# Performance work log

Hardware: AMD Instinct MI355X
Metric: run time of the kernel (lower is better)

The kernel has to match this reference:

```python
import jax, jax.numpy as jnp
import numpy as np

INF = 100000.0
B, W, T, U, S, N = 64, 16, 64, 128, 20, 8


def setup_inputs() -> dict:
    key = jax.random.key(0)
    ks = jax.random.split(key, 9)
    xavier = (2.0 / (U + U)) ** 0.5
    return {
        "slot_utt_h": jax.random.normal(ks[0], (B, W, T, U), jnp.float32),
        "slot_candidate_c": jax.random.normal(ks[1], (S, U), jnp.float32),
        "status_candidate_c": jax.random.normal(ks[2], (N, U), jnp.float32),
        "position_encoding": jax.random.normal(ks[3], (B, W, S, U), jnp.float32),
        "q_status": jax.random.normal(ks[4], (B, W, N, U), jnp.float32),
        "mask": jnp.zeros((B, W, S * N), jnp.float32),
        "weight": jax.random.normal(ks[5], (U, U), jnp.float32) * xavier,  # bilinear co-attention weight [U,U]
        "W1": jax.random.normal(ks[6], (2 * U, U), jnp.float32) * 0.05,
        "b1": jnp.zeros((U,), jnp.float32),
        "W2": jax.random.normal(ks[7], (U, U), jnp.float32) * 0.05,
        "b2": jnp.zeros((U,), jnp.float32),
        "W3": jax.random.normal(ks[8], (U, 1), jnp.float32) * 0.05,
        "b3": jnp.zeros((1,), jnp.float32),
    }


def _zero_mask(p):
    # original: -(p == 0).float() * INF, added before softmax
    return jnp.where(p == 0.0, -INF, 0.0)


def reference(slot_utt_h, slot_candidate_c, status_candidate_c, position_encoding,
              q_status, mask, weight, W1, b1, W2, b2, W3, b3):
    # ---- attention over utterance tokens ----
    # p[b,w,s,t] = <slot_candidate_c[s], slot_utt_h[b,w,t]>
    p = jnp.einsum('su,bwtu->bwst', slot_candidate_c, slot_utt_h)
    p = jax.nn.softmax(p + _zero_mask(p), axis=-1)
    q_slot = jnp.einsum('bwst,bwtu->bwsu', p, slot_utt_h) + position_encoding  # [B,W,S,U]

    # ---- bilinear co-attention: [B,W*S,U] @ weight @ [B,U,W*N] -> [B,W,S,W,N] ----
    co = jnp.einsum('bwsu,uv,bxnv->bwsxn', q_slot, weight, q_status)
    p2 = jax.nn.softmax(co + _zero_mask(co), axis=3)  # softmax over the second window axis x

    # weighted sum of statuses over window axis x
    q_status_slot = jnp.einsum('bwsxn,bxnu->bwsnu', p2, q_status)  # [B,W,S,N,U]

    q_slot_exp = jnp.broadcast_to(q_slot[:, :, :, None, :], (B, W, S, N, U))
    features = jnp.concatenate([q_slot_exp, q_status_slot], axis=-1)  # [B,W,S,N,2U]

    # ---- MLP (dropout in eval mode = identity) ----
    h = jax.nn.relu(features @ W1 + b1)
    h = jax.nn.relu(h @ W2 + b2)
    logits = h @ W3 + b3  # [B,W,S,N,1]

    logits = logits.reshape(B, W, S * N)
    slot_pred_logits = jnp.max(logits + mask, axis=1)  # masked max-pool over window
    slot_pred_labels = (slot_pred_logits > 0.0).astype(jnp.float32)
    return (slot_pred_labels, S * N, slot_pred_logits)
```

## Files before the change

kernel.cpp:

```cpp
#include <hip/hip_runtime.h>
#include <math.h>

#define INF_ 100000.0f
constexpr int B_ = 64, W_ = 16, T_ = 64, U_ = 128, S_ = 20, N_ = 8;

typedef unsigned short ushort_t;
typedef __attribute__((ext_vector_type(8))) short bf16x8;
typedef __attribute__((ext_vector_type(4))) float floatx4;

static __device__ __forceinline__ unsigned short f2bf(float x) {
    unsigned int u = __float_as_uint(x);
    return (unsigned short)((u + 0x7fff + ((u >> 16) & 1)) >> 16);
}
static __device__ __forceinline__ float bf2f(unsigned short s) {
    return __uint_as_float(((unsigned int)s) << 16);
}

#define HT_SWZ(u, t) ((u) * 72 + ((t) ^ ((((u) >> 3) & 7) << 3)))

__global__ __launch_bounds__(256) void k_pre(
    const float* __restrict__ q_status, const float* __restrict__ weight,
    const float* __restrict__ W1, const float* __restrict__ W2,
    const float* __restrict__ c,
    ushort_t* __restrict__ w1topT, ushort_t* __restrict__ w2T,
    ushort_t* __restrict__ c_bf,
    ushort_t* __restrict__ Gt_bf, ushort_t* __restrict__ qs1T_bf)
{
    __shared__ __align__(16) ushort_t sw[128 * 136];
    __shared__ __align__(16) ushort_t sq[128 * 136];
    const int tid = threadIdx.x, bx = blockIdx.x;

    if (bx < 64) {
        const int b = bx;
        const float* qb = q_status + (size_t)b * 16384;
        for (int i = tid * 4; i < 16384; i += 1024) {
            int r = i >> 7, v = i & 127;
            float4 wv = *(const float4*)&weight[i];
            *(ushort4*)&sw[r * 136 + v] =
                (ushort4){f2bf(wv.x), f2bf(wv.y), f2bf(wv.z), f2bf(wv.w)};
            float4 qv = *(const float4*)&qb[i];
            *(ushort4*)&sq[r * 136 + v] =
                (ushort4){f2bf(qv.x), f2bf(qv.y), f2bf(qv.z), f2bf(qv.w)};
        }
        __syncthreads();
        const int wave = tid >> 6, lane = tid & 63, m16 = lane & 15, q = lane >> 4;
        ushort_t* Gb = Gt_bf + (size_t)b * 16384;
#pragma unroll
        for (int ci = 0; ci < 16; ++ci) {
            int tile = wave * 16 + ci;
            int mt = tile >> 3, jt = tile & 7;
            floatx4 acc = {0.f, 0.f, 0.f, 0.f};
#pragma unroll
            for (int kt = 0; kt < 4; ++kt) {
                bf16x8 a = *(const bf16x8*)&sq[(mt * 16 + m16) * 136 + kt * 32 + q * 8];
                bf16x8 w = *(const bf16x8*)&sw[(jt * 16 + m16) * 136 + kt * 32 + q * 8];
                acc = __builtin_amdgcn_mfma_f32_16x16x32_bf16(a, w, acc, 0, 0, 0);
            }
#pragma unroll
            for (int reg = 0; reg < 4; ++reg)
                Gb[(mt * 16 + q * 4 + reg) * 128 + jt * 16 + m16] = f2bf(acc[reg]);
        }
        return;
    }
    if (bx < 128) {
        const int b = bx - 64;
        const float* qb = q_status + (size_t)b * 16384;
        for (int i = tid * 4; i < 16384; i += 1024) {
            int r = i >> 7, v = i & 127;
            float4 qv = *(const float4*)&qb[i];
            *(ushort4*)&sq[r * 136 + v] =
                (ushort4){f2bf(qv.x), f2bf(qv.y), f2bf(qv.z), f2bf(qv.w)};
            int v2 = i >> 7, j = i & 127;
            float4 wv = *(const float4*)&W1[(128 + v2) * 128 + j];
            sw[(j + 0) * 136 + v2] = f2bf(wv.x);
            sw[(j + 1) * 136 + v2] = f2bf(wv.y);
            sw[(j + 2) * 136 + v2] = f2bf(wv.z);
            sw[(j + 3) * 136 + v2] = f2bf(wv.w);
        }
        __syncthreads();
        const int wave = tid >> 6, lane = tid & 63, m16 = lane & 15, q = lane >> 4;
        ushort_t* Qb = qs1T_bf + (size_t)b * 16384;
#pragma unroll
        for (int ci = 0; ci < 16; ++ci) {
            int tile = wave * 16 + ci;
            int mt = tile >> 3, jt = tile & 7;
            floatx4 acc = {0.f, 0.f, 0.f, 0.f};
#pragma unroll
            for (int kt = 0; kt < 4; ++kt) {
                bf16x8 a = *(const bf16x8*)&sq[(mt * 16 + m16) * 136 + kt * 32 + q * 8];
                bf16x8 w = *(const bf16x8*)&sw[(jt * 16 + m16) * 136 + kt * 32 + q * 8];
                acc = __builtin_amdgcn_mfma_f32_16x16x32_bf16(a, w, acc, 0, 0, 0);
            }
            ushort4 o = {f2bf(acc[0]), f2bf(acc[1]), f2bf(acc[2]), f2bf(acc[3])};
            *(ushort4*)&Qb[(jt * 16 + m16) * 128 + mt * 16 + q * 4] = o;
        }
        return;
    }
    if (bx < 144) {
        int g = (bx - 128) * 1024 + tid * 4;
        int j = g >> 7, k = g & 127;
        *(ushort4*)&w1topT[g] =
            (ushort4){f2bf(W1[k * 128 + j]), f2bf(W1[(k + 1) * 128 + j]),
                      f2bf(W1[(k + 2) * 128 + j]), f2bf(W1[(k + 3) * 128 + j])};
        return;
    }
    if (bx < 160) {
        int g = (bx - 144) * 1024 + tid * 4;
        int j = g >> 7, k = g & 127;
        *(ushort4*)&w2T[g] =
            (ushort4){f2bf(W2[k * 128 + j]), f2bf(W2[(k + 1) * 128 + j]),
                      f2bf(W2[(k + 2) * 128 + j]), f2bf(W2[(k + 3) * 128 + j])};
        return;
    }
    for (int i = tid * 4; i < 4096; i += 1024) {
        int s = i >> 7;
        ushort4 o = {0, 0, 0, 0};
        if (s < 20) {
            float4 v = *(const float4*)&c[i];
            o = (ushort4){f2bf(v.x), f2bf(v.y), f2bf(v.z), f2bf(v.w)};
        }
        *(ushort4*)&c_bf[i] = o;
    }
}

__global__ __launch_bounds__(256) void kA(
    const float* __restrict__ h,
    const ushort_t* __restrict__ c_bf,
    const float* __restrict__ pos,
    ushort_t* __restrict__ q_slot_bf)
{
    __shared__ __align__(16) ushort_t sh_hT[128 * 72];
    __shared__ __align__(16) float    sh_sc[32 * 68];
    __shared__ __align__(16) ushort_t sh_P[32 * 72];

    const int bw = blockIdx.x, tid = threadIdx.x;
    const int wave = tid >> 6, lane = tid & 63, m16 = lane & 15, q = lane >> 4;
    const float* hb = h + (size_t)bw * 8192;

    for (int i = tid * 4; i < 8192; i += 1024) {
        int t = i >> 7, u = i & 127;
        float4 v = *(const float4*)&hb[i];
        sh_hT[HT_SWZ(u + 0, t)] = f2bf(v.x);
        sh_hT[HT_SWZ(u + 1, t)] = f2bf(v.y);
        sh_hT[HT_SWZ(u + 2, t)] = f2bf(v.z);
        sh_hT[HT_SWZ(u + 3, t)] = f2bf(v.w);
    }
    for (int i = tid; i < 2304; i += 256) sh_P[i] = 0;

#pragma unroll
    for (int ci = 0; ci < 2; ++ci) {
        int cmb = wave * 2 + ci;
        int mt = cmb >> 2, jt = cmb & 3;
        floatx4 acc = {0.f, 0.f, 0.f, 0.f};
#pragma unroll
        for (int kt = 0; kt < 4; ++kt) {
            bf16x8 a = *(const bf16x8*)&c_bf[(mt * 16 + m16) * 128 + kt * 32 + q * 8];
            const float* hp = &hb[(jt * 16 + m16) * 128 + kt * 32 + q * 8];
            float4 b0 = *(const float4*)&hp[0];
            float4 b1v = *(const float4*)&hp[4];
            bf16x8 bb;
            bb[0] = (short)f2bf(b0.x); bb[1] = (short)f2bf(b0.y);
            bb[2] = (short)f2bf(b0.z); bb[3] = (short)f2bf(b0.w);
            bb[4] = (short)f2bf(b1v.x); bb[5] = (short)f2bf(b1v.y);
            bb[6] = (short)f2bf(b1v.z); bb[7] = (short)f2bf(b1v.w);
            acc = __builtin_amdgcn_mfma_f32_16x16x32_bf16(a, bb, acc, 0, 0, 0);
        }
#pragma unroll
        for (int reg = 0; reg < 4; ++reg)
            sh_sc[(mt * 16 + q * 4 + reg) * 68 + jt * 16 + m16] = acc[reg];
    }
    __syncthreads();

    for (int s = wave; s < 20; s += 4) {
        float v = sh_sc[s * 68 + lane];
        if (v == 0.0f) v = -INF_;
        float m = v;
        for (int d = 32; d; d >>= 1) m = fmaxf(m, __shfl_xor(m, d));
        float e = expf(v - m);
        float sum = e;
        for (int d = 32; d; d >>= 1) sum += __shfl_xor(sum, d);
        sh_P[s * 72 + lane] = f2bf(e / sum);
    }
    __syncthreads();

    const size_t obase = (size_t)bw * 2560;
#pragma unroll
    for (int ci = 0; ci < 4; ++ci) {
        int cmb = wave * 4 + ci;
        int mt = cmb >> 3, jt = cmb & 7;
        floatx4 acc = {0.f, 0.f, 0.f, 0.f};
#pragma unroll
        for (int kt = 0; kt < 2; ++kt) {
            bf16x8 a = *(const bf16x8*)&sh_P[(mt * 16 + m16) * 72 + kt * 32 + q * 8];
            bf16x8 b = *(const bf16x8*)&sh_hT[HT_SWZ(jt * 16 + m16, kt * 32 + q * 8)];
            acc = __builtin_amdgcn_mfma_f32_16x16x32_bf16(a, b, acc, 0, 0, 0);
        }
        int u = jt * 16 + m16;
#pragma unroll
        for (int reg = 0; reg < 4; ++reg) {
            int row = mt * 16 + q * 4 + reg;
            if (row < 20)
                q_slot_bf[obase + row * 128 + u] =
                    f2bf(acc[reg] + pos[obase + row * 128 + u]);
        }
    }
}

__global__ __launch_bounds__(256) void kB(
    const ushort_t* __restrict__ q_slot_bf,
    const ushort_t* __restrict__ Gt_bf,
    const ushort_t* __restrict__ w1topT,
    const float* __restrict__ b1,
    ushort_t* __restrict__ co_bf,
    float* __restrict__ A)
{
    __shared__ __align__(16) ushort_t shB[128 * 136];
    const int tid = threadIdx.x, bx = blockIdx.x;
    const int wave = tid >> 6, lane = tid & 63, m16 = lane & 15, q = lane >> 4;

    if (bx < 320) {
        const int b = bx / 5, rt = bx - b * 5;
        for (int i = tid * 4; i < 16384; i += 1024)
            *(ushort4*)&shB[(i >> 7) * 136 + (i & 127)] =
                *(const ushort4*)&Gt_bf[(size_t)b * 16384 + i];
        __syncthreads();

        const size_t rbase = (size_t)b * 320 + rt * 64 + wave * 16;
        floatx4 acc[8];
#pragma unroll
        for (int jt = 0; jt < 8; ++jt) acc[jt] = (floatx4){0.f, 0.f, 0.f, 0.f};
#pragma unroll
        for (int kt = 0; kt < 4; ++kt) {
            bf16x8 a = *(const bf16x8*)&q_slot_bf[(rbase + m16) * 128 + kt * 32 + q * 8];
#pragma unroll
            for (int jt = 0; jt < 8; ++jt) {
                bf16x8 g = *(const bf16x8*)&shB[(jt * 16 + m16) * 136 + kt * 32 + q * 8];
                acc[jt] = __builtin_amdgcn_mfma_f32_16x16x32_bf16(a, g, acc[jt], 0, 0, 0);
            }
        }
#pragma unroll
        for (int jt = 0; jt < 8; ++jt)
#pragma unroll
            for (int reg = 0; reg < 4; ++reg)
                co_bf[(rbase + q * 4 + reg) * 128 + jt * 16 + m16] = f2bf(acc[jt][reg]);
    } else {
        const int blk = bx - 320;
        for (int i = tid * 4; i < 16384; i += 1024)
            *(ushort4*)&shB[(i >> 7) * 136 + (i & 127)] =
                *(const ushort4*)&w1topT[i];
        __syncthreads();

        const size_t rbase = (size_t)blk * 64 + wave * 16;
        floatx4 acc[8];
#pragma unroll
        for (int jt = 0; jt < 8; ++jt) acc[jt] = (floatx4){0.f, 0.f, 0.f, 0.f};
#pragma unroll
        for (int kt = 0; kt < 4; ++kt) {
            bf16x8 a = *(const bf16x8*)&q_slot_bf[(rbase + m16) * 128 + kt * 32 + q * 8];
#pragma unroll
            for (int jt = 0; jt < 8; ++jt) {
                bf16x8 g = *(const bf16x8*)&shB[(jt * 16 + m16) * 136 + kt * 32 + q * 8];
                acc[jt] = __builtin_amdgcn_mfma_f32_16x16x32_bf16(a, g, acc[jt], 0, 0, 0);
            }
        }
#pragma unroll
        for (int jt = 0; jt < 8; ++jt) {
            int col = jt * 16 + m16;
            float bv = b1[col];
#pragma unroll
            for (int reg = 0; reg < 4; ++reg)
                A[(rbase + q * 4 + reg) * 128 + col] = acc[jt][reg] + bv;
        }
    }
}

__global__ __launch_bounds__(640, 5) void kC(
    const ushort_t* __restrict__ co_bf,
    const ushort_t* __restrict__ qs1T_bf,
    const float* __restrict__ A,
    const ushort_t* __restrict__ w2T,
    const float* __restrict__ b2,
    const float* __restrict__ W3,
    const float* __restrict__ b3,
    float* __restrict__ lg)
{
    __shared__ __align__(16) ushort_t shB[128 * 136];
    __shared__ __align__(16) ushort_t shP[20 * 132];

    const int bw = blockIdx.x, b = bw >> 4, tid = threadIdx.x;
    const int wave = tid >> 6, lane = tid & 63, m16 = lane & 15, q = lane >> 4;

    for (int i = tid * 4; i < 16384; i += 2560) {
        int r = i >> 7, k = i & 127;
        *(ushort4*)&shB[r * 136 + k] = *(const ushort4*)&qs1T_bf[(size_t)b * 16384 + i];
    }

    {
        int sn = tid >> 2, xi = tid & 3;
        int s = sn >> 3, n2 = sn & 7;
        const ushort_t* crow = co_bf + ((size_t)bw * 20 + s) * 128;
        float v[4];
        float m = -INFINITY;
#pragma unroll
        for (int j = 0; j < 4; ++j) {
            float t = bf2f(crow[(xi + 4 * j) * 8 + n2]);
            if (t == 0.0f) t = -INF_;
            v[j] = t;
            m = fmaxf(m, t);
        }
        m = fmaxf(m, __shfl_xor(m, 1));
        m = fmaxf(m, __shfl_xor(m, 2));
        float sum = 0.f;
#pragma unroll
        for (int j = 0; j < 4; ++j) { v[j] = expf(v[j] - m); sum += v[j]; }
        sum += __shfl_xor(sum, 1);
        sum += __shfl_xor(sum, 2);
        float r = 1.0f / sum;
#pragma unroll
        for (int j = 0; j < 4; ++j)
            shP[s * 132 + (xi + 4 * j) * 8 + n2] = f2bf(v[j] * r);
    }
    __syncthreads();

    const int n = m16 & 7;
    const int sIdx = wave * 2 + (m16 >> 3);

    floatx4 gacc[8];
#pragma unroll
    for (int mt = 0; mt < 8; ++mt) gacc[mt] = (floatx4){0.f, 0.f, 0.f, 0.f};
#pragma unroll
    for (int kt = 0; kt < 4; ++kt) {
        short pv = (short)shP[sIdx * 132 + kt * 32 + q * 8 + n];
        bf16x8 pf = {0, 0, 0, 0, 0, 0, 0, 0};
        pf[0] = (n == 0) ? pv : (short)0;
        pf[1] = (n == 1) ? pv : (short)0;
        pf[2] = (n == 2) ? pv : (short)0;
        pf[3] = (n == 3) ? pv : (short)0;
        pf[4] = (n == 4) ? pv : (short)0;
        pf[5] = (n == 5) ? pv : (short)0;
        pf[6] = (n == 6) ? pv : (short)0;
        pf[7] = (n == 7) ? pv : (short)0;
#pragma unroll
        for (int mt = 0; mt < 8; ++mt) {
            bf16x8 af = *(const bf16x8*)&shB[(mt * 16 + m16) * 136 + kt * 32 + q * 8];
            gacc[mt] = __builtin_amdgcn_mfma_f32_16x16x32_bf16(af, pf, gacc[mt], 0, 0, 0);
        }
    }

    unsigned int h1u[8][2];
    {
        const float* Ab = A + ((size_t)bw * 20 + sIdx) * 128;
#pragma unroll
        for (int mt = 0; mt < 8; ++mt) {
            int u0 = mt * 16 + q * 4;
            float4 av = *(const float4*)&Ab[u0];
            unsigned int x0 = f2bf(fmaxf(gacc[mt][0] + av.x, 0.f));
            unsigned int x1 = f2bf(fmaxf(gacc[mt][1] + av.y, 0.f));
            unsigned int x2 = f2bf(fmaxf(gacc[mt][2] + av.z, 0.f));
            unsigned int x3 = f2bf(fmaxf(gacc[mt][3] + av.w, 0.f));
            h1u[mt][0] = x0 | (x1 << 16);
            h1u[mt][1] = x2 | (x3 << 16);
        }
    }
    __syncthreads();

    for (int i = tid * 4; i < 16384; i += 2560) {
        int r = i >> 7, k = i & 127;
        *(ushort4*)&shB[r * 136 + k] = *(const ushort4*)&w2T[i];
    }
    __syncthreads();

    floatx4 acc[8];
#pragma unroll
    for (int jt = 0; jt < 8; ++jt) acc[jt] = (floatx4){0.f, 0.f, 0.f, 0.f};

    const int sl0 = m16 + 16 * ((2 * q) & 3);
    const int sl1 = m16 + 16 * ((2 * q + 1) & 3);
    const bool hi = (q & 2);
#pragma unroll
    for (int kt = 0; kt < 4; ++kt) {
        int wa0 = __shfl((int)h1u[kt * 2 + 0][0], sl0);
        int wb0 = __shfl((int)h1u[kt * 2 + 1][0], sl0);
        int wa1 = __shfl((int)h1u[kt * 2 + 0][1], sl0);
        int wb1 = __shfl((int)h1u[kt * 2 + 1][1], sl0);
        int wa2 = __shfl((int)h1u[kt * 2 + 0][0], sl1);
        int wb2 = __shfl((int)h1u[kt * 2 + 1][0], sl1);
        int wa3 = __shfl((int)h1u[kt * 2 + 0][1], sl1);
        int wb3 = __shfl((int)h1u[kt * 2 + 1][1], sl1);
        int4 fr;
        fr.x = hi ? wb0 : wa0;
        fr.y = hi ? wb1 : wa1;
        fr.z = hi ? wb2 : wa2;
        fr.w = hi ? wb3 : wa3;
        bf16x8 af2 = *(bf16x8*)&fr;
        const int k0 = kt * 32 + q * 8;
#pragma unroll
        for (int jt = 0; jt < 8; ++jt) {
            bf16x8 bfr = *(const bf16x8*)&shB[(jt * 16 + m16) * 136 + k0];
            acc[jt] = __builtin_amdgcn_mfma_f32_16x16x32_bf16(af2, bfr, acc[jt], 0, 0, 0);
        }
    }

    float b2v[8], w3v[8];
#pragma unroll
    for (int jt = 0; jt < 8; ++jt) {
        b2v[jt] = b2[jt * 16 + m16];
        w3v[jt] = W3[jt * 16 + m16];
    }
    const float b3v = b3[0];
#pragma unroll
    for (int reg = 0; reg < 4; ++reg) {
        float p = 0.f;
#pragma unroll
        for (int jt = 0; jt < 8; ++jt)
            p += fmaxf(acc[jt][reg] + b2v[jt], 0.f) * w3v[jt];
        p += __shfl_xor(p, 1);
        p += __shfl_xor(p, 2);
        p += __shfl_xor(p, 4);
        p += __shfl_xor(p, 8);
        if (m16 == 0)
            lg[(size_t)bw * 160 + wave * 16 + q * 4 + reg] = p + b3v;
    }
}

__global__ __launch_bounds__(256) void k5_final(
    const float* __restrict__ lg,
    const float* __restrict__ mask,
    float* __restrict__ out)
{
    int idx = blockIdx.x * 256 + threadIdx.x;
    const int SN = S_ * N_;
    if (idx < B_ * SN) {
        int b = idx / SN, sn = idx % SN;
        float m = -INFINITY;
        for (int w = 0; w < W_; ++w) {
            float v = lg[((size_t)b * W_ + w) * SN + sn] + mask[((size_t)b * W_ + w) * SN + sn];
            m = fmaxf(m, v);
        }
        out[idx] = (m > 0.f) ? 1.f : 0.f;
        out[B_ * SN + 1 + idx] = m;
    }
    if (idx == 0) out[B_ * SN] = (float)SN;
}

extern "C" void kernel_launch(void* const* d_in, const int* in_sizes, int n_in,
                              void* d_out, int out_size, void* d_ws, size_t ws_size,
                              hipStream_t stream) {
    const float* slot_utt_h = (const float*)d_in[0];
    const float* slot_candidate_c = (const float*)d_in[1];
    const float* position_encoding = (const float*)d_in[3];
    const float* q_status = (const float*)d_in[4];
    const float* mask = (const float*)d_in[5];
    const float* weight = (const float*)d_in[6];
    const float* W1 = (const float*)d_in[7];
    const float* b1 = (const float*)d_in[8];
    const float* W2 = (const float*)d_in[9];
    const float* b2 = (const float*)d_in[10];
    const float* W3 = (const float*)d_in[11];
    const float* b3 = (const float*)d_in[12];
    float* out = (float*)d_out;

    float* f = (float*)d_ws;
    float*    lg        = f + 0;
    float*    A         = f + 163840;
    ushort_t* q_slot_bf = (ushort_t*)(f + 2785280);
    ushort_t* co_bf     = (ushort_t*)(f + 4096000);
    ushort_t* Gt_bf     = (ushort_t*)(f + 5406720);
    ushort_t* qs1T_bf   = (ushort_t*)(f + 5931008);
    ushort_t* w1topT    = (ushort_t*)(f + 6455296);
    ushort_t* w2T       = (ushort_t*)(f + 6463488);
    ushort_t* c_bf      = (ushort_t*)(f + 6471680);

    k_pre<<<161, 256, 0, stream>>>(q_status, weight, W1, W2,
                                   slot_candidate_c,
                                   w1topT, w2T, c_bf, Gt_bf, qs1T_bf);
    kA<<<1024, 256, 0, stream>>>(slot_utt_h, c_bf, position_encoding, q_slot_bf);
    kB<<<640, 256, 0, stream>>>(q_slot_bf, Gt_bf, w1topT, b1, co_bf, A);
    kC<<<1024, 640, 0, stream>>>(co_bf, qs1T_bf, A, w2T, b2, W3, b3, lg);
    k5_final<<<(B_ * S_ * N_ + 255) / 256, 256, 0, stream>>>(lg, mask, out);
}
```

Measured before the change: 181.4 us.

## Fuse co-attention and W1-top GEMMs into the per-window MLP kernel

Removes the separate kB kernel and computes the co-attention scores and the q_slot·W1top projection inside each (b,w) block of the MLP kernel. The results go to an LDS arena instead of global co_bf and fp32 A buffers. This cuts one launch and the global round trip for those intermediates. In exchange each block reads Gt and w1topT fragments straight from global memory without LDS staging, and wastes MFMA work padding 20 rows to 32. LDS use per block also grows, which may affect occupancy.

```diff
diff --git a/kernel.cpp b/kernel.cpp
--- a/kernel.cpp
+++ b/kernel.cpp
@@ -206,99 +206,68 @@
     }
 }
 
-__global__ __launch_bounds__(256) void kB(
+__global__ __launch_bounds__(640, 5) void kCp(
     const ushort_t* __restrict__ q_slot_bf,
     const ushort_t* __restrict__ Gt_bf,
     const ushort_t* __restrict__ w1topT,
     const float* __restrict__ b1,
-    ushort_t* __restrict__ co_bf,
-    float* __restrict__ A)
-{
-    __shared__ __align__(16) ushort_t shB[128 * 136];
-    const int tid = threadIdx.x, bx = blockIdx.x;
-    const int wave = tid >> 6, lane = tid & 63, m16 = lane & 15, q = lane >> 4;
-
-    if (bx < 320) {
-        const int b = bx / 5, rt = bx - b * 5;
-        for (int i = tid * 4; i < 16384; i += 1024)
-            *(ushort4*)&shB[(i >> 7) * 136 + (i & 127)] =
-                *(const ushort4*)&Gt_bf[(size_t)b * 16384 + i];
-        __syncthreads();
-
-        const size_t rbase = (size_t)b * 320 + rt * 64 + wave * 16;
-        floatx4 acc[8];
-#pragma unroll
-        for (int jt = 0; jt < 8; ++jt) acc[jt] = (floatx4){0.f, 0.f, 0.f, 0.f};
-#pragma unroll
-        for (int kt = 0; kt < 4; ++kt) {
-            bf16x8 a = *(const bf16x8*)&q_slot_bf[(rbase + m16) * 128 + kt * 32 + q * 8];
-#pragma unroll
-            for (int jt = 0; jt < 8; ++jt) {
-                bf16x8 g = *(const bf16x8*)&shB[(jt * 16 + m16) * 136 + kt * 32 + q * 8];
-                acc[jt] = __builtin_amdgcn_mfma_f32_16x16x32_bf16(a, g, acc[jt], 0, 0, 0);
-            }
-        }
-#pragma unroll
-        for (int jt = 0; jt < 8; ++jt)
-#pragma unroll
-            for (int reg = 0; reg < 4; ++reg)
-                co_bf[(rbase + q * 4 + reg) * 128 + jt * 16 + m16] = f2bf(acc[jt][reg]);
-    } else {
-        const int blk = bx - 320;
-        for (int i = tid * 4; i < 16384; i += 1024)
-            *(ushort4*)&shB[(i >> 7) * 136 + (i & 127)] =
-                *(const ushort4*)&w1topT[i];
-        __syncthreads();
-
-        const size_t rbase = (size_t)blk * 64 + wave * 16;
-        floatx4 acc[8];
-#pragma unroll
-        for (int jt = 0; jt < 8; ++jt) acc[jt] = (floatx4){0.f, 0.f, 0.f, 0.f};
-#pragma unroll
-        for (int kt = 0; kt < 4; ++kt) {
-            bf16x8 a = *(const bf16x8*)&q_slot_bf[(rbase + m16) * 128 + kt * 32 + q * 8];
-#pragma unroll
-            for (int jt = 0; jt < 8; ++jt) {
-                bf16x8 g = *(const bf16x8*)&shB[(jt * 16 + m16) * 136 + kt * 32 + q * 8];
-                acc[jt] = __builtin_amdgcn_mfma_f32_16x16x32_bf16(a, g, acc[jt], 0, 0, 0);
-            }
-        }
-#pragma unroll
-        for (int jt = 0; jt < 8; ++jt) {
-            int col = jt * 16 + m16;
-            float bv = b1[col];
-#pragma unroll
-            for (int reg = 0; reg < 4; ++reg)
-                A[(rbase + q * 4 + reg) * 128 + col] = acc[jt][reg] + bv;
-        }
-    }
-}
-
-__global__ __launch_bounds__(640, 5) void kC(
-    const ushort_t* __restrict__ co_bf,
     const ushort_t* __restrict__ qs1T_bf,
-    const float* __restrict__ A,
     const ushort_t* __restrict__ w2T,
     const float* __restrict__ b2,
     const float* __restrict__ W3,
     const float* __restrict__ b3,
     float* __restrict__ lg)
 {
-    __shared__ __align__(16) ushort_t shB[128 * 136];
-    __shared__ __align__(16) ushort_t shP[20 * 132];
+    __shared__ __align__(16) ushort_t arena[25328];
+    float* Af = (float*)(arena + 20048);
 
     const int bw = blockIdx.x, b = bw >> 4, tid = threadIdx.x;
     const int wave = tid >> 6, lane = tid & 63, m16 = lane & 15, q = lane >> 4;
+    const bf16x8 zz = {0, 0, 0, 0, 0, 0, 0, 0};
 
     for (int i = tid * 4; i < 16384; i += 2560) {
         int r = i >> 7, k = i & 127;
-        *(ushort4*)&shB[r * 136 + k] = *(const ushort4*)&qs1T_bf[(size_t)b * 16384 + i];
-    }
+        *(ushort4*)&arena[r * 136 + k] = *(const ushort4*)&qs1T_bf[(size_t)b * 16384 + i];
+    }
+    {
+        const ushort_t* qsl = q_slot_bf + (size_t)bw * 2560;
+        const ushort_t* Gb = Gt_bf + (size_t)b * 16384;
+        for (int t = wave; t < 32; t += 10) {
+            int isA = t >> 4, tt = t & 15;
+            int mt = tt >> 3, jt = tt & 7;
+            int arow = mt * 16 + m16;
+            const ushort_t* Bsrc = isA ? w1topT : Gb;
+            floatx4 acc = {0.f, 0.f, 0.f, 0.f};
+#pragma unroll
+            for (int kt = 0; kt < 4; ++kt) {
+                bf16x8 a = (arow < 20)
+                    ? *(const bf16x8*)&qsl[arow * 128 + kt * 32 + q * 8] : zz;
+                bf16x8 g = *(const bf16x8*)&Bsrc[(jt * 16 + m16) * 128 + kt * 32 + q * 8];
+                acc = __builtin_amdgcn_mfma_f32_16x16x32_bf16(a, g, acc, 0, 0, 0);
+            }
+            int col = jt * 16 + m16;
+            if (isA) {
+                float bv = b1[col];
+#pragma unroll
+                for (int reg = 0; reg < 4; ++reg) {
+                    int row = mt * 16 + q * 4 + reg;
+                    if (row < 20) Af[row * 132 + col] = acc[reg] + bv;
+                }
+            } else {
+#pragma unroll
+                for (int reg = 0; reg < 4; ++reg) {
+                    int row = mt * 16 + q * 4 + reg;
+                    if (row < 20) arena[17408 + row * 132 + col] = f2bf(acc[reg]);
+                }
+            }
+        }
+    }
+    __syncthreads();
 
     {
         int sn = tid >> 2, xi = tid & 3;
         int s = sn >> 3, n2 = sn & 7;
-        const ushort_t* crow = co_bf + ((size_t)bw * 20 + s) * 128;
+        const ushort_t* crow = &arena[17408 + s * 132];
         float v[4];
         float m = -INFINITY;
 #pragma unroll
@@ -316,9 +285,10 @@
         sum += __shfl_xor(sum, 1);
         sum += __shfl_xor(sum, 2);
         float r = 1.0f / sum;
+        __syncthreads();
 #pragma unroll
         for (int j = 0; j < 4; ++j)
-            shP[s * 132 + (xi + 4 * j) * 8 + n2] = f2bf(v[j] * r);
+            arena[17408 + s * 132 + (xi + 4 * j) * 8 + n2] = f2bf(v[j] * r);
     }
     __syncthreads();
 
@@ -330,7 +300,7 @@
     for (int mt = 0; mt < 8; ++mt) gacc[mt] = (floatx4){0.f, 0.f, 0.f, 0.f};
 #pragma unroll
     for (int kt = 0; kt < 4; ++kt) {
-        short pv = (short)shP[sIdx * 132 + kt * 32 + q * 8 + n];
+        short pv = (short)arena[17408 + sIdx * 132 + kt * 32 + q * 8 + n];
         bf16x8 pf = {0, 0, 0, 0, 0, 0, 0, 0};
         pf[0] = (n == 0) ? pv : (short)0;
         pf[1] = (n == 1) ? pv : (short)0;
@@ -342,14 +312,14 @@
         pf[7] = (n == 7) ? pv : (short)0;
 #pragma unroll
         for (int mt = 0; mt < 8; ++mt) {
-            bf16x8 af = *(const bf16x8*)&shB[(mt * 16 + m16) * 136 + kt * 32 + q * 8];
+            bf16x8 af = *(const bf16x8*)&arena[(mt * 16 + m16) * 136 + kt * 32 + q * 8];
             gacc[mt] = __builtin_amdgcn_mfma_f32_16x16x32_bf16(af, pf, gacc[mt], 0, 0, 0);
         }
     }
 
     unsigned int h1u[8][2];
     {
-        const float* Ab = A + ((size_t)bw * 20 + sIdx) * 128;
+        const float* Ab = Af + sIdx * 132;
 #pragma unroll
         for (int mt = 0; mt < 8; ++mt) {
             int u0 = mt * 16 + q * 4;
@@ -366,7 +336,7 @@
 
     for (int i = tid * 4; i < 16384; i += 2560) {
         int r = i >> 7, k = i & 127;
-        *(ushort4*)&shB[r * 136 + k] = *(const ushort4*)&w2T[i];
+        *(ushort4*)&arena[r * 136 + k] = *(const ushort4*)&w2T[i];
     }
     __syncthreads();
 
@@ -396,7 +366,7 @@
         const int k0 = kt * 32 + q * 8;
 #pragma unroll
         for (int jt = 0; jt < 8; ++jt) {
-            bf16x8 bfr = *(const bf16x8*)&shB[(jt * 16 + m16) * 136 + k0];
+            bf16x8 bfr = *(const bf16x8*)&arena[(jt * 16 + m16) * 136 + k0];
             acc[jt] = __builtin_amdgcn_mfma_f32_16x16x32_bf16(af2, bfr, acc[jt], 0, 0, 0);
         }
     }
@@ -462,20 +432,18 @@
 
     float* f = (float*)d_ws;
     float*    lg        = f + 0;
-    float*    A         = f + 163840;
-    ushort_t* q_slot_bf = (ushort_t*)(f + 2785280);
-    ushort_t* co_bf     = (ushort_t*)(f + 4096000);
-    ushort_t* Gt_bf     = (ushort_t*)(f + 5406720);
-    ushort_t* qs1T_bf   = (ushort_t*)(f + 5931008);
-    ushort_t* w1topT    = (ushort_t*)(f + 6455296);
-    ushort_t* w2T       = (ushort_t*)(f + 6463488);
-    ushort_t* c_bf      = (ushort_t*)(f + 6471680);
+    ushort_t* q_slot_bf = (ushort_t*)(f + 163840);
+    ushort_t* Gt_bf     = (ushort_t*)(f + 1474560);
+    ushort_t* qs1T_bf   = (ushort_t*)(f + 1998848);
+    ushort_t* w1topT    = (ushort_t*)(f + 2523136);
+    ushort_t* w2T       = (ushort_t*)(f + 2531328);
+    ushort_t* c_bf      = (ushort_t*)(f + 2539520);
 
     k_pre<<<161, 256, 0, stream>>>(q_status, weight, W1, W2,
                                    slot_candidate_c,
                                    w1topT, w2T, c_bf, Gt_bf, qs1T_bf);
     kA<<<1024, 256, 0, stream>>>(slot_utt_h, c_bf, position_encoding, q_slot_bf);
-    kB<<<640, 256, 0, stream>>>(q_slot_bf, Gt_bf, w1topT, b1, co_bf, A);
-    kC<<<1024, 640, 0, stream>>>(co_bf, qs1T_bf, A, w2T, b2, W3, b3, lg);
+    kCp<<<1024, 640, 0, stream>>>(q_slot_bf, Gt_bf, w1topT, b1, qs1T_bf,
+                                  w2T, b2, W3, b3, lg);
     k5_final<<<(B_ * S_ * N_ + 255) / 256, 256, 0, stream>>>(lg, mask, out);
 }
```

Result: slower. 201.5 us (+11.1%).
